# Optimization experiments

Measured on AMD Instinct MI355X. Metric: run time of the kernel, lower is better.

## Reference

```python
import jax, jax.numpy as jnp
import numpy as np

B, P, N, C = 4, 12, 1024, 64  # batch, past window, nodes, channels (in==hidden==out)


def setup_inputs() -> dict:
    key = jax.random.key(0)
    k1, k2, k3, k4, k5, k6 = jax.random.split(key, 6)
    x = jax.random.normal(k1, (B, P, N, C), dtype=jnp.float32)
    # float adjacency mask in {0,1}; force self-loops so no softmax row is empty
    A = jax.random.randint(k2, (B, P, N, N), 0, 2).astype(jnp.float32)
    A = A.at[..., jnp.arange(N), jnp.arange(N)].set(1.0)
    # learned params (nn.Linear stores weight as [out, in]; y = x @ W.T)
    W_emb = jax.random.normal(k3, (C, C), dtype=jnp.float32) / jnp.sqrt(jnp.float32(C))
    a1 = jax.random.normal(k4, (C,), dtype=jnp.float32)
    a2 = jax.random.normal(k5, (C,), dtype=jnp.float32)
    W_lin = jax.random.normal(k6, (C, C), dtype=jnp.float32) / jnp.sqrt(jnp.float32(C))
    return {"x": x, "A": A, "W_emb": W_emb, "a1": a1, "a2": a2, "W_lin": W_lin}


def reference(x, A, W_emb, a1, a2, W_lin):
    # x_emb = emb(x)  (bias-free linear)
    x_emb = jnp.einsum('bpnc,hc->bpnh', x, W_emb)            # [B,P,N,H]
    s1 = x_emb @ a1                                           # [B,P,N]
    s2 = x_emb @ a2                                           # [B,P,N]
    # additive GAT scores: a1_i + a2_j, broadcast instead of repeat
    z = jax.nn.leaky_relu(s1[..., :, None] + s2[..., None, :], 0.01)  # [B,P,N,N]
    z = jnp.where(A == 0.0, -jnp.inf, z)
    pi = jax.nn.softmax(z, axis=-1)                           # masked attention
    agg = jnp.einsum('bpij,bpjc->bpic', pi, x)                # weighted aggregation
    out = jax.nn.sigmoid(jnp.einsum('bpic,oc->bpio', agg, W_lin))
    return (out, A)
```

## Files before the change

kernel.cpp:

```cpp
#include <hip/hip_runtime.h>

typedef __attribute__((ext_vector_type(8))) __bf16 bf16x8;
typedef __attribute__((ext_vector_type(4))) float f32x4;

#define N_ 1024
#define C_ 64
#define BP_ 48

static __device__ __forceinline__ unsigned short f2bf(float f) {
    __bf16 b = (__bf16)f;
    return __builtin_bit_cast(unsigned short, b);
}
static __device__ __forceinline__ unsigned int pack2(float a, float b) {
    return (unsigned int)f2bf(a) | ((unsigned int)f2bf(b) << 16);
}

__global__ __launch_bounds__(256) void gat_pre(
    const float* __restrict__ x, const float* __restrict__ Wemb,
    const float* __restrict__ a1, const float* __restrict__ a2,
    float* __restrict__ s1g, float* __restrict__ s2g,
    unsigned short* __restrict__ xP, float* __restrict__ M2part)
{
    __shared__ float xs[64][65];
    __shared__ float vs[2][64];
    const int t = threadIdx.x, l = t & 63, w = t >> 6;
    const int j0 = blockIdx.x * 64;
    const int bp = blockIdx.y;

    if (w == 0) {
        float v1 = 0.f, v2 = 0.f;
        #pragma unroll 8
        for (int h = 0; h < 64; ++h) {
            float we = Wemb[h * 64 + l];
            v1 = fmaf(a1[h], we, v1);
            v2 = fmaf(a2[h], we, v2);
        }
        vs[0][l] = v1; vs[1][l] = v2;
    }
    const float* xb = x + ((size_t)bp * N_ + j0) * C_;
    #pragma unroll
    for (int it = 0; it < 16; ++it)
        xs[it * 4 + w][l] = xb[(it * 4 + w) * C_ + l];
    __syncthreads();

    const int jr = t >> 2, c0 = (t & 3) * 16;
    float p1 = 0.f, p2 = 0.f;
    #pragma unroll
    for (int k = 0; k < 16; ++k) {
        float xv = xs[jr][c0 + k];
        p1 = fmaf(xv, vs[0][c0 + k], p1);
        p2 = fmaf(xv, vs[1][c0 + k], p2);
    }
    p1 += __shfl_xor(p1, 1); p1 += __shfl_xor(p1, 2);
    p2 += __shfl_xor(p2, 1); p2 += __shfl_xor(p2, 2);
    if ((l & 3) == 0) {
        s1g[bp * N_ + j0 + jr] = p1;
        s2g[bp * N_ + j0 + jr] = p2;
    }
    float m = p2;
    m = fmaxf(m, __shfl_xor(m, 4));
    m = fmaxf(m, __shfl_xor(m, 8));
    m = fmaxf(m, __shfl_xor(m, 16));
    m = fmaxf(m, __shfl_xor(m, 32));
    if (l == 0) M2part[bp * 64 + blockIdx.x * 4 + w] = m;

    const int c = t >> 2, part = t & 3;
    unsigned short* dstb = xP + (size_t)bp * C_ * N_ + (size_t)c * N_ + j0 +
                           (part >> 1) * 32 + (part & 1) * 4;
    #pragma unroll
    for (int m_ = 0; m_ < 4; ++m_) {
        unsigned int lo = pack2(xs[part * 16 + 4 * m_ + 0][c],
                                xs[part * 16 + 4 * m_ + 1][c]);
        unsigned int hi = pack2(xs[part * 16 + 4 * m_ + 2][c],
                                xs[part * 16 + 4 * m_ + 3][c]);
        *(uint2*)&dstb[m_ * 8] = make_uint2(lo, hi);
    }
}

__global__ __launch_bounds__(256, 3) void gat_fused(
    const float* __restrict__ Ag, float* __restrict__ outA,
    const unsigned short* __restrict__ xP,
    const float* __restrict__ s1g, const float* __restrict__ s2g,
    const float* __restrict__ M2part,
    const float* __restrict__ Wlin, float* __restrict__ out)
{
    __shared__ unsigned short aggLDS[4][16][72];
    __shared__ float s2lds[1024];
    __shared__ float lsLDS[4][16];

    const int t = threadIdx.x, l = t & 63, w = t >> 6;
    const int i15 = l & 15, q = l >> 4;
    const int bp = blockIdx.y;
    const int ibase = blockIdx.x * 64 + w * 16;

    *(f32x4*)&s2lds[4 * t] = *(const f32x4*)&s2g[bp * N_ + 4 * t];

    float m2v = M2part[bp * 64 + l];
    #pragma unroll
    for (int off = 32; off >= 1; off >>= 1)
        m2v = fmaxf(m2v, __shfl_xor(m2v, off));
    const float M2 = m2v;
    const float s1_l = s1g[bp * N_ + ibase + i15];
    const float zr = s1_l + M2;
    const float mv = fmaxf(zr, 0.01f * zr);

    __syncthreads();

    const float* Arow = Ag + ((size_t)bp * N_ + ibase + i15) * N_ + q * 4;
    float* oArow = outA + ((size_t)bp * N_ + ibase + i15) * N_ + q * 4;
    const unsigned short* xProw = xP + (size_t)bp * C_ * N_ + (size_t)i15 * N_ + q * 8;

    f32x4 acc[4] = {};
    float ls = 0.f;

    f32x4 Aa[4], Ab[4];
    bf16x8 X[8];

#define LOADX(kk) do {                                                        \
    _Pragma("unroll")                                                         \
    for (int nt = 0; nt < 4; ++nt)                                            \
        _Pragma("unroll")                                                     \
        for (int s = 0; s < 2; ++s)                                           \
            X[s * 4 + nt] = *(const bf16x8*)&xProw[(size_t)nt * 16 * N_ +     \
                                                   (kk) * 64 + s * 32];       \
    } while (0)

#define LOADA(Ax, kk) do {                                                    \
    const float* _p = Arow + (kk) * 64;                                       \
    _Pragma("unroll")                                                         \
    for (int g = 0; g < 4; ++g)                                               \
        Ax[g] = __builtin_nontemporal_load((const f32x4*)(_p + g * 16));      \
    } while (0)

#define CONSUME(Ac, kk) do {                                                  \
    const int jrel = (kk) * 64;                                               \
                        \
    f32x4 Ev[4];                                                              \
    _Pragma("unroll")                                                         \
    for (int g = 0; g < 4; ++g) {                                             \
        const f32x4 s2v = *(const f32x4*)&s2lds[jrel + g * 16 + q * 4];       \
        _Pragma("unroll")                                                     \
        for (int r = 0; r < 4; ++r) {                                         \
            float zz = s1_l + s2v[r];                                         \
            zz = fmaxf(zz, 0.01f * zz);                                       \
            Ev[g][r] = __expf(zz - mv);                                       \
        }                                                                     \
    }                                                                         \
                \
    _Pragma("unroll")                                                         \
    for (int g = 0; g < 4; ++g)                                               \
        __builtin_nontemporal_store(Ac[g], (f32x4*)(oArow + jrel + g * 16));  \
    f32x4 P[4];                                                               \
    _Pragma("unroll")                                                         \
    for (int g = 0; g < 4; ++g) {                                             \
        _Pragma("unroll")                                                     \
        for (int r = 0; r < 4; ++r) {                                         \
            P[g][r] = Ac[g][r] * Ev[g][r];                                    \
            ls += P[g][r];                                                    \
        }                                                                     \
    }                                                                         \
    uint4 u0 = make_uint4(pack2(P[0][0], P[0][1]), pack2(P[0][2], P[0][3]),   \
                          pack2(P[1][0], P[1][1]), pack2(P[1][2], P[1][3]));  \
    uint4 u1 = make_uint4(pack2(P[2][0], P[2][1]), pack2(P[2][2], P[2][3]),   \
                          pack2(P[3][0], P[3][1]), pack2(P[3][2], P[3][3]));  \
    bf16x8 af0 = __builtin_bit_cast(bf16x8, u0);                              \
    bf16x8 af1 = __builtin_bit_cast(bf16x8, u1);                              \
    _Pragma("unroll")                                                         \
    for (int nt = 0; nt < 4; ++nt)                                            \
        acc[nt] = __builtin_amdgcn_mfma_f32_16x16x32_bf16(af0, X[nt],         \
                                                          acc[nt], 0, 0, 0);  \
    _Pragma("unroll")                                                         \
    for (int nt = 0; nt < 4; ++nt)                                            \
        acc[nt] = __builtin_amdgcn_mfma_f32_16x16x32_bf16(af1, X[4 + nt],     \
                                                          acc[nt], 0, 0, 0);  \
    } while (0)

    LOADA(Aa, 0);
    #pragma unroll 1
    for (int k = 0; k < 16; k += 2) {
        LOADX(k);
        LOADA(Ab, k + 1);
        CONSUME(Aa, k);
        LOADX(k + 1);
        if (k + 2 < 16) LOADA(Aa, k + 2);
        CONSUME(Ab, k + 1);
    }
#undef LOADX
#undef LOADA
#undef CONSUME

    ls += __shfl_xor(ls, 16);
    ls += __shfl_xor(ls, 32);
    if (q == 0) lsLDS[w][i15] = ls;
    const f32x4 lsq = *(const f32x4*)&lsLDS[w][4 * q];

    unsigned short* aggl = &aggLDS[w][0][0];
    #pragma unroll
    for (int nt = 0; nt < 4; ++nt)
        #pragma unroll
        for (int r = 0; r < 4; ++r)
            aggl[(q * 4 + r) * 72 + nt * 16 + i15] = f2bf(acc[nt][r] / lsq[r]);

    f32x4 d2[4] = {};
    #pragma unroll
    for (int s = 0; s < 2; ++s) {
        bf16x8 af = *(const bf16x8*)&aggl[i15 * 72 + s * 32 + q * 8];
        #pragma unroll
        for (int nt = 0; nt < 4; ++nt) {
            const float* wp = Wlin + (size_t)(nt * 16 + i15) * C_ + s * 32 + q * 8;
            f32x4 w0 = *(const f32x4*)wp;
            f32x4 w1 = *(const f32x4*)(wp + 4);
            bf16x8 bfr;
            #pragma unroll
            for (int jj = 0; jj < 4; ++jj) { bfr[jj] = (__bf16)w0[jj]; bfr[4 + jj] = (__bf16)w1[jj]; }
            d2[nt] = __builtin_amdgcn_mfma_f32_16x16x32_bf16(af, bfr, d2[nt], 0, 0, 0);
        }
    }
    float* orow = out + ((size_t)bp * N_ + ibase) * C_;
    #pragma unroll
    for (int nt = 0; nt < 4; ++nt)
        #pragma unroll
        for (int r = 0; r < 4; ++r)
            orow[(size_t)(q * 4 + r) * C_ + nt * 16 + i15] =
                1.f / (1.f + __expf(-d2[nt][r]));
}

extern "C" void kernel_launch(void* const* d_in, const int* in_sizes, int n_in,
                              void* d_out, int out_size, void* d_ws, size_t ws_size,
                              hipStream_t stream) {
    const float* x    = (const float*)d_in[0];
    const float* Ag   = (const float*)d_in[1];
    const float* Wemb = (const float*)d_in[2];
    const float* a1   = (const float*)d_in[3];
    const float* a2   = (const float*)d_in[4];
    const float* Wlin = (const float*)d_in[5];
    float* out  = (float*)d_out;
    float* outA = out + (size_t)BP_ * N_ * C_;

    float* s1g = (float*)d_ws;
    float* s2g = s1g + BP_ * N_;
    float* M2part = s2g + BP_ * N_;
    unsigned short* xP = (unsigned short*)(M2part + BP_ * 64);

    gat_pre<<<dim3(16, BP_), dim3(256), 0, stream>>>(x, Wemb, a1, a2,
                                                     s1g, s2g, xP, M2part);
    gat_fused<<<dim3(16, BP_), dim3(256), 0, stream>>>(Ag, outA, xP, s1g, s2g,
                                                       M2part, Wlin, out);
}
```

Baseline: 417.7 us.

## Double-buffer x tiles alongside A with sched barriers in fused GAT loop

Result: faster. 396.0 us (-5.2%).

```diff
diff --git a/kernel.cpp b/kernel.cpp
--- a/kernel.cpp
+++ b/kernel.cpp
@@ -77,6 +77,8 @@
     }
 }
 
+#define SB() __builtin_amdgcn_sched_barrier(0)
+
 __global__ __launch_bounds__(256, 3) void gat_fused(
     const float* __restrict__ Ag, float* __restrict__ outA,
     const unsigned short* __restrict__ xP,
@@ -114,27 +116,27 @@
     float ls = 0.f;
 
     f32x4 Aa[4], Ab[4];
-    bf16x8 X[8];
-
-#define LOADX(kk) do {                                                        \
+    bf16x8 Xa[8], Xb[8];
+
+#define LOADX(Xc, kk) do {                                                    \
     _Pragma("unroll")                                                         \
     for (int nt = 0; nt < 4; ++nt)                                            \
         _Pragma("unroll")                                                     \
         for (int s = 0; s < 2; ++s)                                           \
-            X[s * 4 + nt] = *(const bf16x8*)&xProw[(size_t)nt * 16 * N_ +     \
-                                                   (kk) * 64 + s * 32];       \
+            Xc[s * 4 + nt] = *(const bf16x8*)&xProw[(size_t)nt * 16 * N_ +    \
+                                                    (kk) * 64 + s * 32];      \
     } while (0)
 
 #define LOADA(Ax, kk) do {                                                    \
     const float* _p = Arow + (kk) * 64;                                       \
     _Pragma("unroll")                                                         \
     for (int g = 0; g < 4; ++g)                                               \
-        Ax[g] = __builtin_nontemporal_load((const f32x4*)(_p + g * 16));      \
+        Ax[g] = *(const f32x4*)(_p + g * 16);                                 \
     } while (0)
 
-#define CONSUME(Ac, kk) do {                                                  \
+#define CONSUME(Ac, Xc, kk) do {                                              \
     const int jrel = (kk) * 64;                                               \
-                        \
+    \
     f32x4 Ev[4];                                                              \
     _Pragma("unroll")                                                         \
     for (int g = 0; g < 4; ++g) {                                             \
@@ -146,13 +148,12 @@
             Ev[g][r] = __expf(zz - mv);                                       \
         }                                                                     \
     }                                                                         \
-                \
-    _Pragma("unroll")                                                         \
-    for (int g = 0; g < 4; ++g)                                               \
-        __builtin_nontemporal_store(Ac[g], (f32x4*)(oArow + jrel + g * 16));  \
+    SB();                                                                     \
+            \
     f32x4 P[4];                                                               \
     _Pragma("unroll")                                                         \
     for (int g = 0; g < 4; ++g) {                                             \
+        *(f32x4*)(oArow + jrel + g * 16) = Ac[g];                             \
         _Pragma("unroll")                                                     \
         for (int r = 0; r < 4; ++r) {                                         \
             P[g][r] = Ac[g][r] * Ev[g][r];                                    \
@@ -167,24 +168,27 @@
     bf16x8 af1 = __builtin_bit_cast(bf16x8, u1);                              \
     _Pragma("unroll")                                                         \
     for (int nt = 0; nt < 4; ++nt)                                            \
-        acc[nt] = __builtin_amdgcn_mfma_f32_16x16x32_bf16(af0, X[nt],         \
+        acc[nt] = __builtin_amdgcn_mfma_f32_16x16x32_bf16(af0, Xc[nt],        \
                                                           acc[nt], 0, 0, 0);  \
     _Pragma("unroll")                                                         \
     for (int nt = 0; nt < 4; ++nt)                                            \
-        acc[nt] = __builtin_amdgcn_mfma_f32_16x16x32_bf16(af1, X[4 + nt],     \
+        acc[nt] = __builtin_amdgcn_mfma_f32_16x16x32_bf16(af1, Xc[4 + nt],    \
                                                           acc[nt], 0, 0, 0);  \
     } while (0)
 
-    LOADA(Aa, 0);
+    LOADX(Xa, 0); LOADA(Aa, 0);
     #pragma unroll 1
     for (int k = 0; k < 16; k += 2) {
-        LOADX(k);
-        LOADA(Ab, k + 1);
-        CONSUME(Aa, k);
-        LOADX(k + 1);
-        if (k + 2 < 16) LOADA(Aa, k + 2);
-        CONSUME(Ab, k + 1);
-    }
+        SB();
+        LOADX(Xb, k + 1); LOADA(Ab, k + 1);
+        SB();
+        CONSUME(Aa, Xa, k);
+        SB();
+        if (k + 2 < 16) { LOADX(Xa, k + 2); LOADA(Aa, k + 2); }
+        SB();
+        CONSUME(Ab, Xb, k + 1);
+    }
+    SB();
 #undef LOADX
 #undef LOADA
 #undef CONSUME
```
